# Kernel optimization log

Hardware: AMD Instinct MI355X
Metric: run time of the kernel (lower is better)

## Reference

```python
import jax, jax.numpy as jnp
import numpy as np

N_ATOMS = 65536
N_PAIRS = N_ATOMS * 32
MAXZ = 95          # D3 tables cover H..Pu, indexed directly by atomic number
NREF = 5           # number of reference coordination numbers per element
CUTOFF, CUTON = 12.0, 10.0   # model units; distances_model2Bohr == 1
K1, K3 = 16.0, -4.0
SMALL = 1e-30      # fp32 stand-in for the original's 1e-300 double guard


def setup_inputs() -> dict:
    key = jax.random.key(0)
    k0, k1, k2, k3 = jax.random.split(key, 4)
    rng = np.random.default_rng(0)

    atomic_numbers = jax.random.randint(k0, (N_ATOMS,), 1, 87)
    idx_i = jax.random.randint(k1, (N_PAIRS,), 0, N_ATOMS)
    idx_j = jax.random.randint(k2, (N_PAIRS,), 0, N_ATOMS)
    # pair distances spanning inside/switch/outside of the 10..12 cutoff band
    distances = jax.random.uniform(k3, (N_PAIRS,), minval=0.8, maxval=12.5)

    # synthetic stand-ins for the grimme_d3 data files
    rcov = jnp.asarray(rng.uniform(0.5, 3.0, (MAXZ,)).astype(np.float32))
    rcn_np = rng.uniform(0.0, 5.0, (MAXZ, NREF)).astype(np.float32)
    rcn_np[::3, NREF - 1] = -1.0  # mimic -1 padding for missing references
    rcn = jnp.asarray(rcn_np)
    rc6 = jnp.asarray(rng.uniform(1.0, 50.0, (MAXZ, MAXZ, NREF, NREF)).astype(np.float32))
    r2r4 = jnp.asarray(rng.uniform(1.0, 10.0, (MAXZ,)).astype(np.float32))

    s6 = jnp.float32(1.0)
    s8 = jnp.float32(0.9171)
    a1 = jnp.float32(0.3385)
    a2 = jnp.float32(2.883)
    return dict(distances=distances, rcov=rcov, rcn=rcn, rc6=rc6, r2r4=r2r4,
                s6=s6, s8=s8, a1=a1, a2=a2,
                atomic_numbers=atomic_numbers, idx_i=idx_i, idx_j=idx_j)


def reference(distances, rcov, rcn, rc6, r2r4, s6, s8, a1, a2,
              atomic_numbers, idx_i, idx_j):
    n = atomic_numbers.shape[0]
    zi = atomic_numbers[idx_i]
    zj = atomic_numbers[idx_j]

    # smooth switch-off from 1 (r < cuton) to 0 (r >= cutoff)
    x = (CUTOFF - distances) / (CUTOFF - CUTON)
    sw = jnp.where(distances < CUTON, 1.0,
                   jnp.where(distances >= CUTOFF, 0.0,
                             ((6.0 * x - 15.0) * x + 10.0) * x * x * x))

    # coordination numbers via inverse damping, scatter-summed per atom i
    rcov_ij = rcov[zi] + rcov[zj]
    cn_ij = sw / (1.0 + jnp.exp(-K1 * (rcov_ij / distances - 1.0)))
    cn = jax.ops.segment_sum(cn_ij, idx_i, num_segments=n)  # [N]

    # Gaussian weights over reference CNs (soft retrieval into rc6 table)
    rcn_a = rcn[atomic_numbers]                 # [N, NREF]
    mask = rcn_a >= 0
    dcn = rcn_a - cn[:, None]
    gw = jnp.where(mask, jnp.exp(K3 * dcn * dcn), 0.0)
    norm = jnp.sum(gw, axis=-1, keepdims=True)
    # exceptional case: all gaussians underflow -> pick the max reference CN
    rcn_max_a = jnp.max(rcn, axis=-1)[atomic_numbers][:, None]
    exceptional = (rcn_a == rcn_max_a).astype(gw.dtype)
    weights = jnp.where(norm == 0, exceptional, gw / jnp.maximum(norm, SMALL))  # [N, NREF]

    # weighted pairwise C6 from reference table rc6[Zi, Zj, a, b]
    w_i = weights[idx_i]                         # [P, NREF]
    w_j = weights[idx_j]                         # [P, NREF]
    c6 = jnp.einsum('pa,pb,pab->p', w_i, w_j, rc6[zi, zj])

    # C8 = 3 * C6 * <r2>/<r4>_i * <r2>/<r4>_j ; BJ critical radius
    qq = 3.0 * r2r4[zi] * r2r4[zj]
    rr = a1 * jnp.sqrt(qq) + a2

    d2 = distances * distances
    d6 = d2 * d2 * d2
    d8 = d6 * d2
    rr2 = rr * rr
    rr6 = rr2 * rr2 * rr2
    rr8 = rr6 * rr2

    # BJ-damped dispersion energy per pair (0.5 for double counting), switched
    e_pair = -0.5 * (s6 * c6 / (d6 + rr6) + s8 * qq * c6 / (d8 + rr8)) * sw

    # per-atom dispersion energies (energies_Hartree2model == 1)
    return jax.ops.segment_sum(e_pair, idx_i, num_segments=n)
```

## Files before the change

kernel.cpp:

```cpp
#include <hip/hip_runtime.h>
#include <stdint.h>


typedef unsigned short u16;
#define MAXZ 95
#define NREF 5
#define EXC_CUT -87.33654f
#define NB    1024
#define BSH   6
#define BSZ   64
#define CAPSH 12
#define SBLOCKS 128
#define RC_TOTAL (MAXZ * MAXZ * 32)

__device__ __forceinline__ float h2f(u16 h) {
    union { _Float16 h; u16 u; } v; v.u = h; return (float)v.h;
}
__device__ __forceinline__ u16 f2h(float f) {
    union { _Float16 h; u16 u; } v; v.h = (_Float16)f; return v.u;
}

__device__ __forceinline__ float switch_fn(float d) {
    if (d < 10.0f) return 1.0f;
    float x = (12.0f - d) * 0.5f;
    return ((6.0f * x - 15.0f) * x + 10.0f) * x * x * x;
}

__device__ __forceinline__ void calc_weights(const float* __restrict__ rcn_z,
                                             float cni, float* __restrict__ w) {
    float r[NREF], arg[NREF];
    float rmax = -1e30f, marg = -1e30f;
#pragma unroll
    for (int a = 0; a < NREF; a++) {
        r[a] = rcn_z[a];
        rmax = fmaxf(rmax, r[a]);
        float dc = r[a] - cni;
        arg[a] = (-4.0f * dc) * dc;
        if (r[a] >= 0.0f) marg = fmaxf(marg, arg[a]);
    }
    if (marg < EXC_CUT) {
#pragma unroll
        for (int a = 0; a < NREF; a++) w[a] = (r[a] == rmax) ? 1.0f : 0.0f;
    } else {
        float g[NREF], norm = 0.0f;
#pragma unroll
        for (int a = 0; a < NREF; a++) {
            float e = (r[a] >= 0.0f) ? expf(arg[a]) : 0.0f;
            g[a] = e;
            norm += e;
        }
        float inv = 1.0f / fmaxf(norm, 1e-30f);
#pragma unroll
        for (int a = 0; a < NREF; a++) w[a] = g[a] * inv;
    }
}

__global__ __launch_bounds__(1024) void scatter_pairs(const float* __restrict__ dist,
                                                      const int* __restrict__ idx_i,
                                                      const int* __restrict__ idx_j,
                                                      const int* __restrict__ Z,
                                                      const float* __restrict__ rcov,
                                                      const float* __restrict__ rc6,
                                                      float* __restrict__ rcovA,
                                                      u16* __restrict__ rc6pad,
                                                      uint32_t* __restrict__ bcount,
                                                      uint2* __restrict__ recs,
                                                      int n_pairs, int n_atoms,
                                                      int chunk) {
    __shared__ uint32_t hist[NB];
    __shared__ uint32_t run[NB];

    int g = blockIdx.x * 1024 + (int)threadIdx.x;
    int T = gridDim.x * 1024;
    for (int i = g; i < n_atoms; i += T) rcovA[i] = rcov[Z[i]];
    for (int id = g; id < RC_TOTAL; id += T) {
        int tile = id >> 5, slot = id & 31;
        rc6pad[id] = (slot < 25) ? f2h(rc6[(size_t)tile * 25 + slot]) : (u16)0;
    }

    for (int t = threadIdx.x; t < NB; t += 1024) hist[t] = 0;
    __syncthreads();
    int lo = blockIdx.x * chunk;
    int hi = min(lo + chunk, n_pairs);

    for (int q0 = lo + (int)threadIdx.x * 4; q0 < hi; q0 += 4096) {
        int m = min(4, hi - q0);
        float d4[4];
        int i4[4];
        if (m == 4) {
            float4 dv = *(const float4*)(dist + q0);
            int4 iv = *(const int4*)(idx_i + q0);
            d4[0] = dv.x; d4[1] = dv.y; d4[2] = dv.z; d4[3] = dv.w;
            i4[0] = iv.x; i4[1] = iv.y; i4[2] = iv.z; i4[3] = iv.w;
        } else {
            for (int s = 0; s < m; s++) { d4[s] = dist[q0 + s]; i4[s] = idx_i[q0 + s]; }
        }
#pragma unroll
        for (int s = 0; s < 4; s++) {
            if (s < m && d4[s] < 12.0f)
                atomicAdd(&hist[((uint32_t)i4[s]) >> BSH], 1u);
        }
    }
    __syncthreads();
    for (int t = threadIdx.x; t < NB; t += 1024) {
        uint32_t h = hist[t];
        run[t] = h ? atomicAdd(&bcount[t], h) : 0u;
    }
    __syncthreads();

    for (int q0 = lo + (int)threadIdx.x * 4; q0 < hi; q0 += 4096) {
        int m = min(4, hi - q0);
        float d4[4];
        int i4[4], j4[4];
        if (m == 4) {
            float4 dv = *(const float4*)(dist + q0);
            int4 iv = *(const int4*)(idx_i + q0);
            int4 jv = *(const int4*)(idx_j + q0);
            d4[0] = dv.x; d4[1] = dv.y; d4[2] = dv.z; d4[3] = dv.w;
            i4[0] = iv.x; i4[1] = iv.y; i4[2] = iv.z; i4[3] = iv.w;
            j4[0] = jv.x; j4[1] = jv.y; j4[2] = jv.z; j4[3] = jv.w;
        } else {
            for (int s = 0; s < m; s++) {
                d4[s] = dist[q0 + s]; i4[s] = idx_i[q0 + s]; j4[s] = idx_j[q0 + s];
            }
        }
#pragma unroll
        for (int s = 0; s < 4; s++) {
            if (s >= m) continue;
            float d = d4[s];
            if (d >= 12.0f) continue;
            uint32_t i = (uint32_t)i4[s];
            uint32_t b = i >> BSH;
            uint32_t pos = atomicAdd(&run[b], 1u);
            if (pos < (1u << CAPSH)) {
                uint32_t packed = ((uint32_t)j4[s] & 0xFFFFu) |
                                  ((i & (BSZ - 1u)) << 16);
                recs[((size_t)b << CAPSH) + pos] = make_uint2(__float_as_uint(d), packed);
            }
        }
    }
}

__global__ __launch_bounds__(256) void cn_weights_bucket(const uint2* __restrict__ recs,
                                                         const uint32_t* __restrict__ bcount,
                                                         const float* __restrict__ rcovA,
                                                         const int* __restrict__ Z,
                                                         const float* __restrict__ rcn,
                                                         const float* __restrict__ r2r4,
                                                         uint4* __restrict__ arec_h,
                                                         int n_atoms) {
    __shared__ float lrc[BSZ];
    __shared__ float acc[BSZ];
    int b = blockIdx.x;
    int base = b << BSH;
    if (threadIdx.x < BSZ) {
        int i = base + (int)threadIdx.x;
        lrc[threadIdx.x] = (i < n_atoms) ? rcovA[i] : 0.0f;
        acc[threadIdx.x] = 0.0f;
    }
    __syncthreads();
    uint32_t n = min(bcount[b], 1u << CAPSH);
    const uint2* r0 = recs + ((size_t)b << CAPSH);
    if (n) {
        uint32_t nm1 = n - 1;
        uint32_t k = threadIdx.x;
        uint2 recA = r0[min(k, nm1)];
        uint2 recB = r0[min(k + 256, nm1)];
        float rjA = rcovA[recA.y & 0xFFFF];
        for (; k < n; k += 256) {
            uint2 recC = r0[min(k + 512, nm1)];
            float rjB = rcovA[recB.y & 0xFFFF];
            float d = __uint_as_float(recA.x);
            int il = (recA.y >> 16) & (BSZ - 1);
            float rij = lrc[il] + rjA;
            float sw = switch_fn(d);
            atomicAdd(&acc[il], sw / (1.0f + expf(-16.0f * (rij / d - 1.0f))));
            recA = recB; recB = recC; rjA = rjB;
        }
    }
    __syncthreads();
    if (threadIdx.x < BSZ) {
        int i = base + (int)threadIdx.x;
        if (i < n_atoms) {
            int z = Z[i];
            float w[NREF];
            calc_weights(rcn + (size_t)z * NREF, acc[threadIdx.x], w);
            uint4 pk;
            pk.x = (uint32_t)f2h(w[0]) | ((uint32_t)f2h(w[1]) << 16);
            pk.y = (uint32_t)f2h(w[2]) | ((uint32_t)f2h(w[3]) << 16);
            pk.z = (uint32_t)f2h(w[4]) | ((uint32_t)f2h(r2r4[z]) << 16);
            pk.w = (uint32_t)z;
            arec_h[i] = pk;
        }
    }
}

__global__ __launch_bounds__(256) void energy_bucket(const uint2* __restrict__ recs,
                                                     const uint32_t* __restrict__ bcount,
                                                     const uint4* __restrict__ arec_h,
                                                     const u16* __restrict__ rc6pad,
                                                     const float* __restrict__ s6p,
                                                     const float* __restrict__ s8p,
                                                     const float* __restrict__ a1p,
                                                     const float* __restrict__ a2p,
                                                     float* __restrict__ eout,
                                                     int n_atoms) {
    __shared__ float4 la0[BSZ];
    __shared__ float4 la1[BSZ];
    __shared__ float  acc[BSZ];
    int b = blockIdx.x;
    int base = b << BSH;
    if (threadIdx.x < BSZ) {
        int i = min(base + (int)threadIdx.x, n_atoms - 1);
        uint4 pk = arec_h[i];
        la0[threadIdx.x] = make_float4(h2f(pk.x & 0xFFFFu), h2f(pk.x >> 16),
                                       h2f(pk.y & 0xFFFFu), h2f(pk.y >> 16));
        la1[threadIdx.x] = make_float4(h2f(pk.z & 0xFFFFu), h2f(pk.z >> 16),
                                       __int_as_float((int)pk.w), 0.0f);
        acc[threadIdx.x] = 0.0f;
    }
    __syncthreads();
    float s6 = s6p[0], s8 = s8p[0], a1 = a1p[0], a2 = a2p[0];
    uint32_t n = min(bcount[b], 1u << CAPSH);
    const uint2* r0 = recs + ((size_t)b << CAPSH);
    if (n) {
        uint32_t nm1 = n - 1;
        uint32_t k = threadIdx.x;
        uint2 recA = r0[min(k, nm1)];
        uint2 recB = r0[min(k + 256, nm1)];
        uint4 pjA = arec_h[recA.y & 0xFFFFu];
        for (; k < n; k += 256) {
            uint2 recC = r0[min(k + 512, nm1)];
            uint4 pjB = arec_h[recB.y & 0xFFFFu];

            int il = (recA.y >> 16) & (BSZ - 1);
            float4 ai1 = la1[il];
            int zi = __float_as_int(ai1.z);
            int zj = (int)pjA.w;
            const uint4* T4 = (const uint4*)(rc6pad + (size_t)(zi * MAXZ + zj) * 32);
            uint4 t0 = T4[0], t1 = T4[1], t2 = T4[2];
            uint32_t t3 = ((const uint32_t*)T4)[12];

            float d = __uint_as_float(recA.x);
            float4 ai0 = la0[il];
            float wi[NREF] = {ai0.x, ai0.y, ai0.z, ai0.w, ai1.x};
            float wj[NREF] = {h2f(pjA.x & 0xFFFFu), h2f(pjA.x >> 16),
                              h2f(pjA.y & 0xFFFFu), h2f(pjA.y >> 16),
                              h2f(pjA.z & 0xFFFFu)};
            float r2r4j = h2f(pjA.z >> 16);

            float tt[25];
            uint32_t tw[12] = {t0.x, t0.y, t0.z, t0.w, t1.x, t1.y, t1.z, t1.w,
                               t2.x, t2.y, t2.z, t2.w};
#pragma unroll
            for (int k2 = 0; k2 < 12; k2++) {
                tt[2 * k2]     = h2f((u16)(tw[k2] & 0xFFFFu));
                tt[2 * k2 + 1] = h2f((u16)(tw[k2] >> 16));
            }
            tt[24] = h2f((u16)(t3 & 0xFFFFu));

            float c6 = 0.0f;
#pragma unroll
            for (int a = 0; a < NREF; a++) {
                float ss = 0.0f;
#pragma unroll
                for (int bb = 0; bb < NREF; bb++) ss = fmaf(wj[bb], tt[a * NREF + bb], ss);
                c6 = fmaf(wi[a], ss, c6);
            }

            float qq = 3.0f * ai1.y * r2r4j;
            float rr = a1 * sqrtf(qq) + a2;
            float d2 = d * d;
            float d6 = d2 * d2 * d2;
            float d8 = d6 * d2;
            float rr2 = rr * rr;
            float rr6 = rr2 * rr2 * rr2;
            float rr8 = rr6 * rr2;
            float sw = switch_fn(d);

            float e = -0.5f * (s6 * c6 / (d6 + rr6) + s8 * qq * c6 / (d8 + rr8)) * sw;
            atomicAdd(&acc[il], e);

            recA = recB; recB = recC; pjA = pjB;
        }
    }
    __syncthreads();
    if (threadIdx.x < BSZ) {
        int i = base + (int)threadIdx.x;
        if (i < n_atoms) eout[i] = acc[threadIdx.x];
    }
}

__global__ __launch_bounds__(256) void pair_cn_slim(const float* __restrict__ dist,
                                                    const float* __restrict__ rcov,
                                                    const int* __restrict__ Z,
                                                    const int* __restrict__ idx_i,
                                                    const int* __restrict__ idx_j,
                                                    float* __restrict__ cn,
                                                    int n_pairs) {
    int p = blockIdx.x * blockDim.x + threadIdx.x;
    if (p >= n_pairs) return;
    float d = dist[p];
    if (d >= 12.0f) return;
    float rij = rcov[Z[idx_i[p]]] + rcov[Z[idx_j[p]]];
    float sw = switch_fn(d);
    atomicAdd(&cn[idx_i[p]], sw / (1.0f + expf(-16.0f * (rij / d - 1.0f))));
}

__global__ __launch_bounds__(256) void pair_energy_slim(const float* __restrict__ dist,
                                                        const int* __restrict__ Z,
                                                        const int* __restrict__ idx_i,
                                                        const int* __restrict__ idx_j,
                                                        const float* __restrict__ cn,
                                                        const float* __restrict__ rcn,
                                                        const float* __restrict__ r2r4,
                                                        const float* __restrict__ rc6,
                                                        const float* __restrict__ s6p,
                                                        const float* __restrict__ s8p,
                                                        const float* __restrict__ a1p,
                                                        const float* __restrict__ a2p,
                                                        float* __restrict__ eout,
                                                        int n_pairs) {
    int p = blockIdx.x * blockDim.x + threadIdx.x;
    if (p >= n_pairs) return;
    float d = dist[p];
    if (d >= 12.0f) return;
    int i = idx_i[p], j = idx_j[p];
    int zi = Z[i], zj = Z[j];
    float wi[NREF], wj[NREF];
    calc_weights(rcn + (size_t)zi * NREF, cn[i], wi);
    calc_weights(rcn + (size_t)zj * NREF, cn[j], wj);
    const float* T = rc6 + (size_t)(zi * MAXZ + zj) * 25;
    float c6 = 0.0f;
#pragma unroll
    for (int a = 0; a < NREF; a++) {
        float s = 0.0f;
#pragma unroll
        for (int bb = 0; bb < NREF; bb++) s = fmaf(wj[bb], T[a * NREF + bb], s);
        c6 = fmaf(wi[a], s, c6);
    }
    float qq = 3.0f * r2r4[zi] * r2r4[zj];
    float rr = a1p[0] * sqrtf(qq) + a2p[0];
    float d2 = d * d;
    float d6 = d2 * d2 * d2;
    float d8 = d6 * d2;
    float rr2 = rr * rr;
    float rr6 = rr2 * rr2 * rr2;
    float rr8 = rr6 * rr2;
    float sw = switch_fn(d);
    float e = -0.5f * (s6p[0] * c6 / (d6 + rr6) + s8p[0] * qq * c6 / (d8 + rr8)) * sw;
    atomicAdd(&eout[i], e);
}

extern "C" void kernel_launch(void* const* d_in, const int* in_sizes, int n_in,
                              void* d_out, int out_size, void* d_ws, size_t ws_size,
                              hipStream_t stream) {
    const float* dist = (const float*)d_in[0];
    const float* rcov = (const float*)d_in[1];
    const float* rcn  = (const float*)d_in[2];
    const float* rc6  = (const float*)d_in[3];
    const float* r2r4 = (const float*)d_in[4];
    const float* s6p  = (const float*)d_in[5];
    const float* s8p  = (const float*)d_in[6];
    const float* a1p  = (const float*)d_in[7];
    const float* a2p  = (const float*)d_in[8];
    const int* Z    = (const int*)d_in[9];
    const int* idxi = (const int*)d_in[10];
    const int* idxj = (const int*)d_in[11];
    float* out = (float*)d_out;

    int n_pairs = in_sizes[0];
    int n_atoms = in_sizes[9];

    char* ws = (char*)d_ws;
    size_t o_bcount = 0;
    size_t o_rcovA  = 4096;
    size_t o_arec   = (o_rcovA + (size_t)n_atoms * 4 + 15) & ~(size_t)15;
    size_t o_rc6    = (o_arec + (size_t)n_atoms * 16 + 63) & ~(size_t)63;
    size_t o_recs   = (o_rc6 + (size_t)RC_TOTAL * 2 + 255) & ~(size_t)255;
    size_t need     = o_recs + ((size_t)NB << CAPSH) * 8;

    uint32_t* bcount = (uint32_t*)(ws + o_bcount);
    float* rcovA  = (float*)(ws + o_rcovA);
    uint4* arec_h = (uint4*)(ws + o_arec);
    u16*   rcpad  = (u16*)(ws + o_rc6);
    uint2* recs   = (uint2*)(ws + o_recs);

    if (ws_size >= need && n_atoms <= NB * BSZ && n_atoms <= 65536) {
        hipMemsetAsync(bcount, 0, NB * 4, stream);
        int chunk = (n_pairs + SBLOCKS - 1) / SBLOCKS;
        scatter_pairs<<<SBLOCKS, 1024, 0, stream>>>(dist, idxi, idxj, Z, rcov, rc6,
                                                    rcovA, rcpad, bcount, recs,
                                                    n_pairs, n_atoms, chunk);
        cn_weights_bucket<<<NB, 256, 0, stream>>>(recs, bcount, rcovA, Z, rcn, r2r4,
                                                  arec_h, n_atoms);
        energy_bucket<<<NB, 256, 0, stream>>>(recs, bcount, arec_h, rcpad,
                                              s6p, s8p, a1p, a2p, out, n_atoms);
    } else {
        int pgrid = (n_pairs + 255) / 256;
        float* cn = (float*)(ws + o_rcovA);
        hipMemsetAsync(out, 0, (size_t)n_atoms * 4, stream);
        hipMemsetAsync(cn, 0, (size_t)n_atoms * 4, stream);
        pair_cn_slim<<<pgrid, 256, 0, stream>>>(dist, rcov, Z, idxi, idxj, cn, n_pairs);
        pair_energy_slim<<<pgrid, 256, 0, stream>>>(dist, Z, idxi, idxj, cn, rcn, r2r4,
                                                    rc6, s6p, s8p, a1p, a2p, out, n_pairs);
    }
}
```

Baseline: 147.8 us.

## Stage bucketed pair records in LDS tiles to coalesce global scatter writes

The pair-scatter kernel now processes each block's chunk in 16K-pair tiles. Each tile is loaded once into registers and histogrammed by bucket, and a block-wide prefix scan gives per-bucket offsets. Records are then sorted into a shared-memory staging buffer and written to global memory in bucket-contiguous runs. This removes the second read pass over dist/idx_i/idx_j and turns scattered 8-byte global writes into mostly contiguous ones. The cost is 128KB of LDS per block, which limits occupancy, plus a 10-step scan with many barriers and one global atomic per bucket per tile instead of per block.

```diff
diff --git a/kernel.cpp b/kernel.cpp
--- a/kernel.cpp
+++ b/kernel.cpp
@@ -11,6 +11,7 @@
 #define BSZ   64
 #define CAPSH 12
 #define SBLOCKS 128
+#define TILE  16384
 #define RC_TOTAL (MAXZ * MAXZ * 32)
 
 __device__ __forceinline__ float h2f(u16 h) {
@@ -67,10 +68,14 @@
                                                       uint2* __restrict__ recs,
                                                       int n_pairs, int n_atoms,
                                                       int chunk) {
+    __shared__ uint2 stage[TILE];
     __shared__ uint32_t hist[NB];
-    __shared__ uint32_t run[NB];
-
-    int g = blockIdx.x * 1024 + (int)threadIdx.x;
+    __shared__ uint32_t startb[NB];
+    __shared__ uint32_t cur[NB];
+    __shared__ uint32_t res[NB];
+
+    int tid = (int)threadIdx.x;
+    int g = blockIdx.x * 1024 + tid;
     int T = gridDim.x * 1024;
     for (int i = g; i < n_atoms; i += T) rcovA[i] = rcov[Z[i]];
     for (int id = g; id < RC_TOTAL; id += T) {
@@ -78,66 +83,84 @@
         rc6pad[id] = (slot < 25) ? f2h(rc6[(size_t)tile * 25 + slot]) : (u16)0;
     }
 
-    for (int t = threadIdx.x; t < NB; t += 1024) hist[t] = 0;
-    __syncthreads();
     int lo = blockIdx.x * chunk;
     int hi = min(lo + chunk, n_pairs);
 
-    for (int q0 = lo + (int)threadIdx.x * 4; q0 < hi; q0 += 4096) {
-        int m = min(4, hi - q0);
-        float d4[4];
-        int i4[4];
-        if (m == 4) {
-            float4 dv = *(const float4*)(dist + q0);
-            int4 iv = *(const int4*)(idx_i + q0);
-            d4[0] = dv.x; d4[1] = dv.y; d4[2] = dv.z; d4[3] = dv.w;
-            i4[0] = iv.x; i4[1] = iv.y; i4[2] = iv.z; i4[3] = iv.w;
-        } else {
-            for (int s = 0; s < m; s++) { d4[s] = dist[q0 + s]; i4[s] = idx_i[q0 + s]; }
-        }
-#pragma unroll
-        for (int s = 0; s < 4; s++) {
-            if (s < m && d4[s] < 12.0f)
-                atomicAdd(&hist[((uint32_t)i4[s]) >> BSH], 1u);
-        }
-    }
-    __syncthreads();
-    for (int t = threadIdx.x; t < NB; t += 1024) {
-        uint32_t h = hist[t];
-        run[t] = h ? atomicAdd(&bcount[t], h) : 0u;
-    }
-    __syncthreads();
-
-    for (int q0 = lo + (int)threadIdx.x * 4; q0 < hi; q0 += 4096) {
-        int m = min(4, hi - q0);
-        float d4[4];
-        int i4[4], j4[4];
-        if (m == 4) {
-            float4 dv = *(const float4*)(dist + q0);
-            int4 iv = *(const int4*)(idx_i + q0);
-            int4 jv = *(const int4*)(idx_j + q0);
-            d4[0] = dv.x; d4[1] = dv.y; d4[2] = dv.z; d4[3] = dv.w;
-            i4[0] = iv.x; i4[1] = iv.y; i4[2] = iv.z; i4[3] = iv.w;
-            j4[0] = jv.x; j4[1] = jv.y; j4[2] = jv.z; j4[3] = jv.w;
-        } else {
-            for (int s = 0; s < m; s++) {
-                d4[s] = dist[q0 + s]; i4[s] = idx_i[q0 + s]; j4[s] = idx_j[q0 + s];
+    for (int t0 = lo; t0 < hi; t0 += TILE) {
+        int tend = min(t0 + TILE, hi);
+        hist[tid] = 0;
+        __syncthreads();
+
+        uint32_t rx[16], ry[16], vm = 0;
+#pragma unroll
+        for (int it = 0; it < 4; it++) {
+            int q0 = t0 + tid * 4 + it * 4096;
+            int m = (q0 < tend) ? min(4, tend - q0) : 0;
+            float d4[4]; int i4[4], j4[4];
+            if (m == 4) {
+                float4 dv = *(const float4*)(dist + q0);
+                int4 iv = *(const int4*)(idx_i + q0);
+                int4 jv = *(const int4*)(idx_j + q0);
+                d4[0] = dv.x; d4[1] = dv.y; d4[2] = dv.z; d4[3] = dv.w;
+                i4[0] = iv.x; i4[1] = iv.y; i4[2] = iv.z; i4[3] = iv.w;
+                j4[0] = jv.x; j4[1] = jv.y; j4[2] = jv.z; j4[3] = jv.w;
+            } else {
+                for (int s = 0; s < m; s++) {
+                    d4[s] = dist[q0 + s]; i4[s] = idx_i[q0 + s]; j4[s] = idx_j[q0 + s];
+                }
             }
-        }
-#pragma unroll
-        for (int s = 0; s < 4; s++) {
-            if (s >= m) continue;
-            float d = d4[s];
-            if (d >= 12.0f) continue;
-            uint32_t i = (uint32_t)i4[s];
-            uint32_t b = i >> BSH;
-            uint32_t pos = atomicAdd(&run[b], 1u);
-            if (pos < (1u << CAPSH)) {
-                uint32_t packed = ((uint32_t)j4[s] & 0xFFFFu) |
-                                  ((i & (BSZ - 1u)) << 16);
-                recs[((size_t)b << CAPSH) + pos] = make_uint2(__float_as_uint(d), packed);
+#pragma unroll
+            for (int s = 0; s < 4; s++) {
+                int k = it * 4 + s;
+                rx[k] = 0u; ry[k] = 0u;
+                if (s < m && d4[s] < 12.0f) {
+                    uint32_t i = (uint32_t)i4[s];
+                    uint32_t b = i >> BSH;
+                    rx[k] = __float_as_uint(d4[s]);
+                    ry[k] = ((uint32_t)j4[s] & 0xFFFFu) |
+                            ((i & (BSZ - 1u)) << 16) | (b << 22);
+                    vm |= (1u << k);
+                    atomicAdd(&hist[b], 1u);
+                }
             }
         }
+        __syncthreads();
+
+        cur[tid] = hist[tid];
+        __syncthreads();
+#pragma unroll
+        for (int off = 1; off < NB; off <<= 1) {
+            uint32_t v = (tid >= off) ? cur[tid - off] : 0u;
+            __syncthreads();
+            cur[tid] += v;
+            __syncthreads();
+        }
+        startb[tid] = cur[tid] - hist[tid];
+        uint32_t h = hist[tid];
+        res[tid] = h ? atomicAdd(&bcount[tid], h) : 0u;
+        cur[tid] = startb[tid];
+        __syncthreads();
+
+#pragma unroll
+        for (int k = 0; k < 16; k++) {
+            if (vm & (1u << k)) {
+                uint32_t b = ry[k] >> 22;
+                uint32_t pos = atomicAdd(&cur[b], 1u);
+                stage[pos] = make_uint2(rx[k], ry[k]);
+            }
+        }
+        __syncthreads();
+
+        uint32_t total = startb[NB - 1] + hist[NB - 1];
+        for (uint32_t t = (uint32_t)tid; t < total; t += 1024u) {
+            uint2 r = stage[t];
+            uint32_t b = r.y >> 22;
+            uint32_t gpos = res[b] + (t - startb[b]);
+            if (gpos < (1u << CAPSH))
+                recs[((size_t)b << CAPSH) + gpos] =
+                    make_uint2(r.x, r.y & 0x3FFFFFu);
+        }
+        __syncthreads();
     }
 }
 
```

Result: faster. 139.0 us, median of 2 (-6.0%).

## Replace bucketed pair scatter with direct global atomics and fixed-point CN sums

Applied to the files above, without the earlier changes.

Drops the bucket-sort pass (histogram, record scatter, per-bucket LDS reduction) and computes CN and energy directly per pair, using global atomics on idx_i. CN is accumulated as scaled 32-bit fixed-point integers so its sum is order-independent. The energy kernel gathers packed per-atom records for both i and j from global memory instead of LDS. This removes one full pass over the pairs and the record buffer, at the cost of many random global atomics, weaker locality, and possible fixed-point overflow or rounding in CN.

```diff
diff --git a/kernel.cpp b/kernel.cpp
--- a/kernel.cpp
+++ b/kernel.cpp
@@ -6,12 +6,9 @@
 #define MAXZ 95
 #define NREF 5
 #define EXC_CUT -87.33654f
-#define NB    1024
-#define BSH   6
-#define BSZ   64
-#define CAPSH 12
-#define SBLOCKS 128
 #define RC_TOTAL (MAXZ * MAXZ * 32)
+#define CN_SCALE 33554432.0f
+#define CN_INV   2.9802322387695312e-8f
 
 __device__ __forceinline__ float h2f(u16 h) {
     union { _Float16 h; u16 u; } v; v.u = h; return (float)v.h;
@@ -55,63 +52,25 @@
     }
 }
 
-__global__ __launch_bounds__(1024) void scatter_pairs(const float* __restrict__ dist,
-                                                      const int* __restrict__ idx_i,
-                                                      const int* __restrict__ idx_j,
-                                                      const int* __restrict__ Z,
-                                                      const float* __restrict__ rcov,
-                                                      const float* __restrict__ rc6,
-                                                      float* __restrict__ rcovA,
-                                                      u16* __restrict__ rc6pad,
-                                                      uint32_t* __restrict__ bcount,
-                                                      uint2* __restrict__ recs,
-                                                      int n_pairs, int n_atoms,
-                                                      int chunk) {
-    __shared__ uint32_t hist[NB];
-    __shared__ uint32_t run[NB];
-
+__global__ __launch_bounds__(1024) void pair_cn_fix(const float* __restrict__ dist,
+                                                    const int* __restrict__ idx_i,
+                                                    const int* __restrict__ idx_j,
+                                                    const int* __restrict__ Z,
+                                                    const float* __restrict__ rcov,
+                                                    const float* __restrict__ rc6,
+                                                    u16* __restrict__ rc6pad,
+                                                    uint32_t* __restrict__ cnfix,
+                                                    int n_pairs) {
     int g = blockIdx.x * 1024 + (int)threadIdx.x;
     int T = gridDim.x * 1024;
-    for (int i = g; i < n_atoms; i += T) rcovA[i] = rcov[Z[i]];
     for (int id = g; id < RC_TOTAL; id += T) {
         int tile = id >> 5, slot = id & 31;
         rc6pad[id] = (slot < 25) ? f2h(rc6[(size_t)tile * 25 + slot]) : (u16)0;
     }
 
-    for (int t = threadIdx.x; t < NB; t += 1024) hist[t] = 0;
-    __syncthreads();
-    int lo = blockIdx.x * chunk;
-    int hi = min(lo + chunk, n_pairs);
-
-    for (int q0 = lo + (int)threadIdx.x * 4; q0 < hi; q0 += 4096) {
-        int m = min(4, hi - q0);
-        float d4[4];
-        int i4[4];
-        if (m == 4) {
-            float4 dv = *(const float4*)(dist + q0);
-            int4 iv = *(const int4*)(idx_i + q0);
-            d4[0] = dv.x; d4[1] = dv.y; d4[2] = dv.z; d4[3] = dv.w;
-            i4[0] = iv.x; i4[1] = iv.y; i4[2] = iv.z; i4[3] = iv.w;
-        } else {
-            for (int s = 0; s < m; s++) { d4[s] = dist[q0 + s]; i4[s] = idx_i[q0 + s]; }
-        }
-#pragma unroll
-        for (int s = 0; s < 4; s++) {
-            if (s < m && d4[s] < 12.0f)
-                atomicAdd(&hist[((uint32_t)i4[s]) >> BSH], 1u);
-        }
-    }
-    __syncthreads();
-    for (int t = threadIdx.x; t < NB; t += 1024) {
-        uint32_t h = hist[t];
-        run[t] = h ? atomicAdd(&bcount[t], h) : 0u;
-    }
-    __syncthreads();
-
-    for (int q0 = lo + (int)threadIdx.x * 4; q0 < hi; q0 += 4096) {
-        int m = min(4, hi - q0);
-        float d4[4];
-        int i4[4], j4[4];
+    for (int q0 = g * 4; q0 < n_pairs; q0 += T * 4) {
+        int m = min(4, n_pairs - q0);
+        float d4[4]; int i4[4], j4[4];
         if (m == 4) {
             float4 dv = *(const float4*)(dist + q0);
             int4 iv = *(const int4*)(idx_i + q0);
@@ -129,125 +88,86 @@
             if (s >= m) continue;
             float d = d4[s];
             if (d >= 12.0f) continue;
-            uint32_t i = (uint32_t)i4[s];
-            uint32_t b = i >> BSH;
-            uint32_t pos = atomicAdd(&run[b], 1u);
-            if (pos < (1u << CAPSH)) {
-                uint32_t packed = ((uint32_t)j4[s] & 0xFFFFu) |
-                                  ((i & (BSZ - 1u)) << 16);
-                recs[((size_t)b << CAPSH) + pos] = make_uint2(__float_as_uint(d), packed);
+            float rij = rcov[Z[i4[s]]] + rcov[Z[j4[s]]];
+            float sw = switch_fn(d);
+            float c = sw / (1.0f + expf(-16.0f * (rij / d - 1.0f)));
+            atomicAdd(&cnfix[i4[s]], __float2uint_rn(c * CN_SCALE));
+        }
+    }
+}
+
+__global__ __launch_bounds__(256) void atom_weights(const uint32_t* __restrict__ cnfix,
+                                                    const int* __restrict__ Z,
+                                                    const float* __restrict__ rcn,
+                                                    const float* __restrict__ r2r4,
+                                                    uint4* __restrict__ arec_h,
+                                                    float* __restrict__ eout,
+                                                    int n_atoms) {
+    int i = blockIdx.x * 256 + (int)threadIdx.x;
+    if (i >= n_atoms) return;
+    float cni = (float)cnfix[i] * CN_INV;
+    int z = Z[i];
+    float w[NREF];
+    calc_weights(rcn + (size_t)z * NREF, cni, w);
+    uint4 pk;
+    pk.x = (uint32_t)f2h(w[0]) | ((uint32_t)f2h(w[1]) << 16);
+    pk.y = (uint32_t)f2h(w[2]) | ((uint32_t)f2h(w[3]) << 16);
+    pk.z = (uint32_t)f2h(w[4]) | ((uint32_t)f2h(r2r4[z]) << 16);
+    pk.w = (uint32_t)z;
+    arec_h[i] = pk;
+    eout[i] = 0.0f;
+}
+
+__global__ __launch_bounds__(256) void pair_energy(const float* __restrict__ dist,
+                                                   const int* __restrict__ idx_i,
+                                                   const int* __restrict__ idx_j,
+                                                   const uint4* __restrict__ arec_h,
+                                                   const u16* __restrict__ rc6pad,
+                                                   const float* __restrict__ s6p,
+                                                   const float* __restrict__ s8p,
+                                                   const float* __restrict__ a1p,
+                                                   const float* __restrict__ a2p,
+                                                   float* __restrict__ eout,
+                                                   int n_pairs) {
+    float s6 = s6p[0], s8 = s8p[0], a1 = a1p[0], a2 = a2p[0];
+    int g = blockIdx.x * 256 + (int)threadIdx.x;
+    int T = gridDim.x * 256;
+    for (int q0 = g * 4; q0 < n_pairs; q0 += T * 4) {
+        int m = min(4, n_pairs - q0);
+        float d4[4]; int i4[4], j4[4];
+        if (m == 4) {
+            float4 dv = *(const float4*)(dist + q0);
+            int4 iv = *(const int4*)(idx_i + q0);
+            int4 jv = *(const int4*)(idx_j + q0);
+            d4[0] = dv.x; d4[1] = dv.y; d4[2] = dv.z; d4[3] = dv.w;
+            i4[0] = iv.x; i4[1] = iv.y; i4[2] = iv.z; i4[3] = iv.w;
+            j4[0] = jv.x; j4[1] = jv.y; j4[2] = jv.z; j4[3] = jv.w;
+        } else {
+            for (int s = 0; s < m; s++) {
+                d4[s] = dist[q0 + s]; i4[s] = idx_i[q0 + s]; j4[s] = idx_j[q0 + s];
             }
         }
-    }
-}
-
-__global__ __launch_bounds__(256) void cn_weights_bucket(const uint2* __restrict__ recs,
-                                                         const uint32_t* __restrict__ bcount,
-                                                         const float* __restrict__ rcovA,
-                                                         const int* __restrict__ Z,
-                                                         const float* __restrict__ rcn,
-                                                         const float* __restrict__ r2r4,
-                                                         uint4* __restrict__ arec_h,
-                                                         int n_atoms) {
-    __shared__ float lrc[BSZ];
-    __shared__ float acc[BSZ];
-    int b = blockIdx.x;
-    int base = b << BSH;
-    if (threadIdx.x < BSZ) {
-        int i = base + (int)threadIdx.x;
-        lrc[threadIdx.x] = (i < n_atoms) ? rcovA[i] : 0.0f;
-        acc[threadIdx.x] = 0.0f;
-    }
-    __syncthreads();
-    uint32_t n = min(bcount[b], 1u << CAPSH);
-    const uint2* r0 = recs + ((size_t)b << CAPSH);
-    if (n) {
-        uint32_t nm1 = n - 1;
-        uint32_t k = threadIdx.x;
-        uint2 recA = r0[min(k, nm1)];
-        uint2 recB = r0[min(k + 256, nm1)];
-        float rjA = rcovA[recA.y & 0xFFFF];
-        for (; k < n; k += 256) {
-            uint2 recC = r0[min(k + 512, nm1)];
-            float rjB = rcovA[recB.y & 0xFFFF];
-            float d = __uint_as_float(recA.x);
-            int il = (recA.y >> 16) & (BSZ - 1);
-            float rij = lrc[il] + rjA;
-            float sw = switch_fn(d);
-            atomicAdd(&acc[il], sw / (1.0f + expf(-16.0f * (rij / d - 1.0f))));
-            recA = recB; recB = recC; rjA = rjB;
-        }
-    }
-    __syncthreads();
-    if (threadIdx.x < BSZ) {
-        int i = base + (int)threadIdx.x;
-        if (i < n_atoms) {
-            int z = Z[i];
-            float w[NREF];
-            calc_weights(rcn + (size_t)z * NREF, acc[threadIdx.x], w);
-            uint4 pk;
-            pk.x = (uint32_t)f2h(w[0]) | ((uint32_t)f2h(w[1]) << 16);
-            pk.y = (uint32_t)f2h(w[2]) | ((uint32_t)f2h(w[3]) << 16);
-            pk.z = (uint32_t)f2h(w[4]) | ((uint32_t)f2h(r2r4[z]) << 16);
-            pk.w = (uint32_t)z;
-            arec_h[i] = pk;
-        }
-    }
-}
-
-__global__ __launch_bounds__(256) void energy_bucket(const uint2* __restrict__ recs,
-                                                     const uint32_t* __restrict__ bcount,
-                                                     const uint4* __restrict__ arec_h,
-                                                     const u16* __restrict__ rc6pad,
-                                                     const float* __restrict__ s6p,
-                                                     const float* __restrict__ s8p,
-                                                     const float* __restrict__ a1p,
-                                                     const float* __restrict__ a2p,
-                                                     float* __restrict__ eout,
-                                                     int n_atoms) {
-    __shared__ float4 la0[BSZ];
-    __shared__ float4 la1[BSZ];
-    __shared__ float  acc[BSZ];
-    int b = blockIdx.x;
-    int base = b << BSH;
-    if (threadIdx.x < BSZ) {
-        int i = min(base + (int)threadIdx.x, n_atoms - 1);
-        uint4 pk = arec_h[i];
-        la0[threadIdx.x] = make_float4(h2f(pk.x & 0xFFFFu), h2f(pk.x >> 16),
-                                       h2f(pk.y & 0xFFFFu), h2f(pk.y >> 16));
-        la1[threadIdx.x] = make_float4(h2f(pk.z & 0xFFFFu), h2f(pk.z >> 16),
-                                       __int_as_float((int)pk.w), 0.0f);
-        acc[threadIdx.x] = 0.0f;
-    }
-    __syncthreads();
-    float s6 = s6p[0], s8 = s8p[0], a1 = a1p[0], a2 = a2p[0];
-    uint32_t n = min(bcount[b], 1u << CAPSH);
-    const uint2* r0 = recs + ((size_t)b << CAPSH);
-    if (n) {
-        uint32_t nm1 = n - 1;
-        uint32_t k = threadIdx.x;
-        uint2 recA = r0[min(k, nm1)];
-        uint2 recB = r0[min(k + 256, nm1)];
-        uint4 pjA = arec_h[recA.y & 0xFFFFu];
-        for (; k < n; k += 256) {
-            uint2 recC = r0[min(k + 512, nm1)];
-            uint4 pjB = arec_h[recB.y & 0xFFFFu];
-
-            int il = (recA.y >> 16) & (BSZ - 1);
-            float4 ai1 = la1[il];
-            int zi = __float_as_int(ai1.z);
-            int zj = (int)pjA.w;
+#pragma unroll
+        for (int s = 0; s < 4; s++) {
+            if (s >= m) continue;
+            float d = d4[s];
+            if (d >= 12.0f) continue;
+            uint4 pi = arec_h[i4[s]];
+            uint4 pj = arec_h[j4[s]];
+            int zi = (int)pi.w;
+            int zj = (int)pj.w;
             const uint4* T4 = (const uint4*)(rc6pad + (size_t)(zi * MAXZ + zj) * 32);
             uint4 t0 = T4[0], t1 = T4[1], t2 = T4[2];
             uint32_t t3 = ((const uint32_t*)T4)[12];
 
-            float d = __uint_as_float(recA.x);
-            float4 ai0 = la0[il];
-            float wi[NREF] = {ai0.x, ai0.y, ai0.z, ai0.w, ai1.x};
-            float wj[NREF] = {h2f(pjA.x & 0xFFFFu), h2f(pjA.x >> 16),
-                              h2f(pjA.y & 0xFFFFu), h2f(pjA.y >> 16),
-                              h2f(pjA.z & 0xFFFFu)};
-            float r2r4j = h2f(pjA.z >> 16);
+            float wi[NREF] = {h2f(pi.x & 0xFFFFu), h2f(pi.x >> 16),
+                              h2f(pi.y & 0xFFFFu), h2f(pi.y >> 16),
+                              h2f(pi.z & 0xFFFFu)};
+            float wj[NREF] = {h2f(pj.x & 0xFFFFu), h2f(pj.x >> 16),
+                              h2f(pj.y & 0xFFFFu), h2f(pj.y >> 16),
+                              h2f(pj.z & 0xFFFFu)};
+            float r2r4i = h2f(pi.z >> 16);
+            float r2r4j = h2f(pj.z >> 16);
 
             float tt[25];
             uint32_t tw[12] = {t0.x, t0.y, t0.z, t0.w, t1.x, t1.y, t1.z, t1.w,
@@ -268,7 +188,7 @@
                 c6 = fmaf(wi[a], ss, c6);
             }
 
-            float qq = 3.0f * ai1.y * r2r4j;
+            float qq = 3.0f * r2r4i * r2r4j;
             float rr = a1 * sqrtf(qq) + a2;
             float d2 = d * d;
             float d6 = d2 * d2 * d2;
@@ -279,15 +199,8 @@
             float sw = switch_fn(d);
 
             float e = -0.5f * (s6 * c6 / (d6 + rr6) + s8 * qq * c6 / (d8 + rr8)) * sw;
-            atomicAdd(&acc[il], e);
-
-            recA = recB; recB = recC; pjA = pjB;
-        }
-    }
-    __syncthreads();
-    if (threadIdx.x < BSZ) {
-        int i = base + (int)threadIdx.x;
-        if (i < n_atoms) eout[i] = acc[threadIdx.x];
+            atomicAdd(&eout[i4[s]], e);
+        }
     }
 }
 
@@ -373,32 +286,27 @@
     int n_atoms = in_sizes[9];
 
     char* ws = (char*)d_ws;
-    size_t o_bcount = 0;
-    size_t o_rcovA  = 4096;
-    size_t o_arec   = (o_rcovA + (size_t)n_atoms * 4 + 15) & ~(size_t)15;
-    size_t o_rc6    = (o_arec + (size_t)n_atoms * 16 + 63) & ~(size_t)63;
-    size_t o_recs   = (o_rc6 + (size_t)RC_TOTAL * 2 + 255) & ~(size_t)255;
-    size_t need     = o_recs + ((size_t)NB << CAPSH) * 8;
-
-    uint32_t* bcount = (uint32_t*)(ws + o_bcount);
-    float* rcovA  = (float*)(ws + o_rcovA);
+    size_t o_cnfix = 0;
+    size_t o_arec  = ((size_t)n_atoms * 4 + 255) & ~(size_t)255;
+    size_t o_rc6   = (o_arec + (size_t)n_atoms * 16 + 63) & ~(size_t)63;
+    size_t need    = o_rc6 + (size_t)RC_TOTAL * 2;
+
+    uint32_t* cnfix = (uint32_t*)(ws + o_cnfix);
     uint4* arec_h = (uint4*)(ws + o_arec);
     u16*   rcpad  = (u16*)(ws + o_rc6);
-    uint2* recs   = (uint2*)(ws + o_recs);
-
-    if (ws_size >= need && n_atoms <= NB * BSZ && n_atoms <= 65536) {
-        hipMemsetAsync(bcount, 0, NB * 4, stream);
-        int chunk = (n_pairs + SBLOCKS - 1) / SBLOCKS;
-        scatter_pairs<<<SBLOCKS, 1024, 0, stream>>>(dist, idxi, idxj, Z, rcov, rc6,
-                                                    rcovA, rcpad, bcount, recs,
-                                                    n_pairs, n_atoms, chunk);
-        cn_weights_bucket<<<NB, 256, 0, stream>>>(recs, bcount, rcovA, Z, rcn, r2r4,
-                                                  arec_h, n_atoms);
-        energy_bucket<<<NB, 256, 0, stream>>>(recs, bcount, arec_h, rcpad,
-                                              s6p, s8p, a1p, a2p, out, n_atoms);
+
+    if (ws_size >= need && n_atoms <= 65536) {
+        hipMemsetAsync(cnfix, 0, (size_t)n_atoms * 4, stream);
+        pair_cn_fix<<<512, 1024, 0, stream>>>(dist, idxi, idxj, Z, rcov, rc6,
+                                              rcpad, cnfix, n_pairs);
+        atom_weights<<<(n_atoms + 255) / 256, 256, 0, stream>>>(cnfix, Z, rcn, r2r4,
+                                                                arec_h, out, n_atoms);
+        int egrid = min((n_pairs / 4 + 255) / 256 + 1, 4096);
+        pair_energy<<<egrid, 256, 0, stream>>>(dist, idxi, idxj, arec_h, rcpad,
+                                               s6p, s8p, a1p, a2p, out, n_pairs);
     } else {
         int pgrid = (n_pairs + 255) / 256;
-        float* cn = (float*)(ws + o_rcovA);
+        float* cn = (float*)(ws + 4096);
         hipMemsetAsync(out, 0, (size_t)n_atoms * 4, stream);
         hipMemsetAsync(cn, 0, (size_t)n_atoms * 4, stream);
         pair_cn_slim<<<pgrid, 256, 0, stream>>>(dist, rcov, Z, idxi, idxj, cn, n_pairs);
```

Result: slower. 286.9 us (+94.1%).
